# Kernel tuning notes

Hardware: AMD Instinct MI355X
Metric: run time of the kernel (lower is better)

## Reference

```python
import jax, jax.numpy as jnp
import numpy as np

NEG_SLOPE = 0.2  # PyG GATConv default negative_slope


def setup_inputs() -> dict:
    key = jax.random.key(0)
    ks = jax.random.split(key, 10)
    B, N, E = 8, 10000, 160000
    Din, Dout = 128, 128
    x = jax.random.normal(ks[0], (B, N, Din), dtype=jnp.float32)
    src = jax.random.randint(ks[1], (E,), 0, N)
    dst = jax.random.randint(ks[2], (E,), 0, N)
    edge_index = jnp.stack([src, dst])  # [2, E]
    edge_attr = jax.random.uniform(ks[3], (E,), dtype=jnp.float32)
    lim = 1.0 / np.sqrt(Din)
    W = jax.random.uniform(ks[4], (Dout, Din), jnp.float32, -lim, lim)   # shared lin (src==dst)
    We = jax.random.uniform(ks[5], (Dout, 1), jnp.float32, -1.0, 1.0)    # lin_edge, edge_dim=1
    att_src = jax.random.normal(ks[6], (Dout,), jnp.float32) * 0.1
    att_dst = jax.random.normal(ks[7], (Dout,), jnp.float32) * 0.1
    att_edge = jax.random.normal(ks[8], (Dout,), jnp.float32) * 0.1
    bias = jnp.zeros((Dout,), jnp.float32)
    return {"x": x, "edge_index": edge_index, "edge_attr": edge_attr,
            "W": W, "We": We, "att_src": att_src, "att_dst": att_dst,
            "att_edge": att_edge, "bias": bias}


def reference(x, edge_index, edge_attr, W, We, att_src, att_dst, att_edge, bias):
    B, N, Din = x.shape
    src, dst = edge_index[0], edge_index[1]
    # --- add self loops with fill_value='mean' (mean of incoming edge_attr per node) ---
    deg = jax.ops.segment_sum(jnp.ones_like(edge_attr), dst, num_segments=N)
    loop_attr = jax.ops.segment_sum(edge_attr, dst, num_segments=N) / jnp.maximum(deg, 1.0)
    ar = jnp.arange(N, dtype=src.dtype)
    full_src = jnp.concatenate([src, ar])          # [E2]
    full_dst = jnp.concatenate([dst, ar])          # [E2]
    full_attr = jnp.concatenate([edge_attr, loop_attr])
    # edge features: Linear(1 -> Dout, no bias) == outer product; identical across batch
    e_feat = full_attr[:, None] * We[:, 0][None, :]        # [E2, Dout]
    alpha_e = e_feat @ att_edge                            # [E2]

    def single(xb):  # xb: [N, Din]
        h = xb @ W.T                                       # [N, Dout]
        a_src = h @ att_src                                # [N]
        a_dst = h @ att_dst                                # [N]
        a = a_src[full_src] + a_dst[full_dst] + alpha_e    # [E2]
        a = jax.nn.leaky_relu(a, NEG_SLOPE)
        # segment softmax over destination node
        a_max = jax.ops.segment_max(a, full_dst, num_segments=N)
        a_max = jnp.where(jnp.isfinite(a_max), a_max, 0.0)
        ex = jnp.exp(a - a_max[full_dst])
        s = jax.ops.segment_sum(ex, full_dst, num_segments=N)
        alpha = ex / (s[full_dst] + 1e-16)                 # [E2]
        out = jax.ops.segment_sum(alpha[:, None] * h[full_src], full_dst, num_segments=N)
        return out + bias, alpha

    x_out, attn = jax.vmap(single)(x)   # [B, N, Dout], [B, E2]
    return x_out, attn
```

## Files before the change

### kernel.cpp

```cpp
#include <hip/hip_runtime.h>
#include <hip/hip_bf16.h>

typedef short short8 __attribute__((ext_vector_type(8)));
typedef float floatx4 __attribute__((ext_vector_type(4)));

static constexpr int BATCH = 8;
static constexpr int NN    = 10000;
static constexpr int EE    = 160000;
static constexpr int EE2   = EE + NN;
static constexpr int DD    = 128;
static constexpr float SLOPE = 0.2f;
static constexpr long OUT_ELEMS = (long)BATCH * NN * DD;
static constexpr int EB = EE / 256;

__device__ inline float ldf(const void* p, long i, int f32) {
    return f32 ? ((const float*)p)[i]
               : __bfloat162float(((const __hip_bfloat16*)p)[i]);
}
__device__ inline int esrc(const int* ei, int e, int i64) { return i64 ? ei[2 * e] : ei[e]; }
__device__ inline int edst(const int* ei, int e, int i64) { return i64 ? ei[2 * (EE + e)] : ei[EE + e]; }
__device__ inline short bf16bits(float v) {
    __hip_bfloat16 b = __float2bfloat16(v);
    short s; __builtin_memcpy(&s, &b, 2); return s;
}

__global__ __launch_bounds__(256) void k_detect(const unsigned short* __restrict__ xu,
                                                const int* __restrict__ ei,
                                                const void* __restrict__ We,
                                                const void* __restrict__ att_edge,
                                                int* __restrict__ flags,
                                                float* __restrict__ cout,
                                                int* __restrict__ deg,
                                                float* __restrict__ lsum) {
    int t = threadIdx.x;
    if (blockIdx.x > 0) {
        int idx = (blockIdx.x - 1) * 256 + t;
        if (idx < NN) { deg[idx] = 0; lsum[idx] = 0.f; }
        return;
    }
    __shared__ int cnt[2];
    __shared__ float red[256];
    if (t < 2) cnt[t] = 0;
    __syncthreads();
    int c1 = 0;
    for (int i = t; i < 32768; i += 256) {
        unsigned short u = xu[i];
        if ((u & 0x7F80u) == 0x7F80u) c1++;
    }
    int c2 = (ei[2 * t + 1] != 0) ? 1 : 0;
    if (c1) atomicAdd(&cnt[0], c1);
    if (c2) atomicAdd(&cnt[1], c2);
    __syncthreads();
    int f32 = (cnt[0] > 0);
    if (t == 0) { flags[0] = f32; flags[1] = (cnt[1] == 0); }
    red[t] = (t < DD) ? ldf(We, t, f32) * ldf(att_edge, t, f32) : 0.f;
    __syncthreads();
    for (int o = 128; o > 0; o >>= 1) {
        if (t < o) red[t] += red[t + o];
        __syncthreads();
    }
    if (t == 0) *cout = red[0];
}

__global__ __launch_bounds__(256) void k_deg(const int* __restrict__ ei,
                                             const void* __restrict__ attr,
                                             const void* __restrict__ W,
                                             const int* __restrict__ flags,
                                             int* __restrict__ deg, float* __restrict__ lsum,
                                             __hip_bfloat16* __restrict__ Wb) {
    int f32 = flags[0], i64 = flags[1];
    int bId = blockIdx.x, t = threadIdx.x;
    if (bId < EB) {
        int e = bId * 256 + t;
        int d = edst(ei, e, i64);
        atomicAdd(&deg[d], 1);
        atomicAdd(&lsum[d], ldf(attr, e, f32));
    } else {
        int idx = (bId - EB) * 512 + t * 2;
        if (f32) {
            float2 v = ((const float2*)W)[idx >> 1];
            Wb[idx]     = __float2bfloat16(v.x);
            Wb[idx + 1] = __float2bfloat16(v.y);
        } else {
            ((ushort2*)Wb)[idx >> 1] = ((const ushort2*)W)[idx >> 1];
        }
    }
}

template<int F32>
__device__ inline void load_a(const void* __restrict__ x, long row, int quad, short8 afr[4]) {
    if (F32) {
        const float* xr = (const float*)x + row * DD;
        #pragma unroll
        for (int kk = 0; kk < 4; kk++) {
            float4 f0 = *(const float4*)(xr + kk * 32 + quad * 8);
            float4 f1 = *(const float4*)(xr + kk * 32 + quad * 8 + 4);
            short8 a;
            a[0] = bf16bits(f0.x); a[1] = bf16bits(f0.y); a[2] = bf16bits(f0.z); a[3] = bf16bits(f0.w);
            a[4] = bf16bits(f1.x); a[5] = bf16bits(f1.y); a[6] = bf16bits(f1.z); a[7] = bf16bits(f1.w);
            afr[kk] = a;
        }
    } else {
        const short* xr = (const short*)x + row * DD;
        #pragma unroll
        for (int kk = 0; kk < 4; kk++)
            afr[kk] = *(const short8*)(xr + kk * 32 + quad * 8);
    }
}

__global__ __launch_bounds__(128) void k_gemm(const void* __restrict__ x,
                                              const __hip_bfloat16* __restrict__ Wb,
                                              const void* __restrict__ att_src,
                                              const void* __restrict__ att_dst,
                                              const int* __restrict__ flags,
                                              __hip_bfloat16* __restrict__ h,
                                              float* __restrict__ asrc_t, float* __restrict__ adst_t) {
    __shared__ float tile[2][16 * 132];
    int f32 = flags[0];
    int wave = threadIdx.x >> 6;
    int lane = threadIdx.x & 63;
    int l15  = lane & 15, quad = lane >> 4;
    long rows_base = (long)blockIdx.x * 32 + wave * 16;

    short8 afr[4];
    if (f32) load_a<1>(x, rows_base + l15, quad, afr);
    else     load_a<0>(x, rows_base + l15, quad, afr);

    const short* wr = (const short*)Wb;
    floatx4 acc[8];
    #pragma unroll
    for (int jt = 0; jt < 8; jt++) acc[jt] = (floatx4){0.f, 0.f, 0.f, 0.f};
    #pragma unroll
    for (int jt = 0; jt < 8; jt++) {
        #pragma unroll
        for (int kk = 0; kk < 4; kk++) {
            short8 bfr = *(const short8*)(wr + (jt * 16 + l15) * DD + kk * 32 + quad * 8);
            acc[jt] = __builtin_amdgcn_mfma_f32_16x16x32_bf16(afr[kk], bfr, acc[jt], 0, 0, 0);
        }
    }

    float asum[4] = {0.f, 0.f, 0.f, 0.f};
    float dsum[4] = {0.f, 0.f, 0.f, 0.f};
    #pragma unroll
    for (int jt = 0; jt < 8; jt++) {
        int col = jt * 16 + l15;
        float as = ldf(att_src, col, f32);
        float ad = ldf(att_dst, col, f32);
        #pragma unroll
        for (int r = 0; r < 4; r++) {
            asum[r] += acc[jt][r] * as;
            dsum[r] += acc[jt][r] * ad;
        }
    }
    #pragma unroll
    for (int r = 0; r < 4; r++) {
        float a = asum[r], d = dsum[r];
        #pragma unroll
        for (int o = 1; o < 16; o <<= 1) { a += __shfl_xor(a, o, 64); d += __shfl_xor(d, o, 64); }
        if (l15 == 0) {
            long row = rows_base + quad * 4 + r;
            int b = (int)(row / NN), n = (int)(row - (long)b * NN);
            asrc_t[n * 8 + b] = a;
            adst_t[n * 8 + b] = d;
        }
    }

    float* tl = &tile[wave][0];
    #pragma unroll
    for (int jt = 0; jt < 8; jt++)
        #pragma unroll
        for (int r = 0; r < 4; r++)
            tl[(quad * 4 + r) * 132 + jt * 16 + l15] = acc[jt][r];
    short* hp = (short*)h;
    #pragma unroll
    for (int it = 0; it < 4; it++) {
        int row = it * 4 + quad;
        float4 f0 = *(const float4*)&tl[row * 132 + l15 * 8];
        float4 f1 = *(const float4*)&tl[row * 132 + l15 * 8 + 4];
        short8 o;
        o[0] = bf16bits(f0.x); o[1] = bf16bits(f0.y); o[2] = bf16bits(f0.z); o[3] = bf16bits(f0.w);
        o[4] = bf16bits(f1.x); o[5] = bf16bits(f1.y); o[6] = bf16bits(f1.z); o[7] = bf16bits(f1.w);
        *(short8*)(hp + (rows_base + row) * DD + l15 * 8) = o;
    }
}

__global__ __launch_bounds__(1024) void k_scan(const int* __restrict__ deg, int* __restrict__ offs) {
    __shared__ int part[1024];
    int t = threadIdx.x;
    const int PER = (NN + 1023) / 1024;
    int base = t * PER;
    int s = 0;
    for (int i = 0; i < PER; i++) { int idx = base + i; if (idx < NN) s += deg[idx]; }
    part[t] = s;
    __syncthreads();
    for (int o = 1; o < 1024; o <<= 1) {
        int v = (t >= o) ? part[t - o] : 0;
        __syncthreads();
        part[t] += v;
        __syncthreads();
    }
    int run = (t == 0) ? 0 : part[t - 1];
    for (int i = 0; i < PER; i++) {
        int idx = base + i;
        if (idx < NN) { offs[idx] = run; run += deg[idx]; }
    }
    if (t == 1023) offs[NN] = run;
}

__global__ __launch_bounds__(256) void k_fill(const int* __restrict__ ei,
                                              const void* __restrict__ attr,
                                              const int* __restrict__ flags,
                                              int* __restrict__ offs,
                                              int* __restrict__ srcs, float* __restrict__ attrs) {
    int f32 = flags[0], i64 = flags[1];
    int e = blockIdx.x * 256 + threadIdx.x;
    if (e < EE) {
        int d = edst(ei, e, i64);
        int s = esrc(ei, e, i64);
        float at = ldf(attr, e, f32);
        int p = atomicAdd(&offs[d], 1);
        srcs[p] = s;
        attrs[p] = at;
    }
}

__global__ __launch_bounds__(256) void k_agg(const int* __restrict__ srcs,
                                             const float* __restrict__ attrs,
                                             const float* __restrict__ asrc_t,
                                             const float* __restrict__ adst_t,
                                             const __hip_bfloat16* __restrict__ h,
                                             const int* __restrict__ deg,
                                             const float* __restrict__ lsum,
                                             const int* __restrict__ offs,
                                             const float* __restrict__ cptr,
                                             const void* __restrict__ bias,
                                             const int* __restrict__ flags,
                                             float* __restrict__ invT,
                                             void* __restrict__ outbuf) {
    int f32 = flags[0];
    int tid = threadIdx.x;
    int g   = (tid & 63) >> 4;
    int c16 = tid & 15;
    int wv  = tid >> 6;
    int b = blockIdx.x & 7;
    int n = (blockIdx.x >> 3) * 16 + wv * 4 + g;

    float c   = *cptr;
    int dg    = deg[n];
    int off   = offs[n] - dg;
    int cnt   = dg + 1;
    float lattr = lsum[n] / fmaxf((float)dg, 1.0f);
    float an  = adst_t[n * 8 + b];

    const unsigned short* hb = (const unsigned short*)h + (long)b * NN * DD;
    float acc[8];
    #pragma unroll
    for (int j = 0; j < 8; j++) acc[j] = 0.f;
    float ssum = 0.f;

    uint4 hvA = {0,0,0,0}, hvB = {0,0,0,0};
    float arA = 0.f, atA = 0.f, arB = 0.f, atB = 0.f;

#define FETCH_EDGE(I, HV, AR, AT)                                   \
    { int _s; if ((I) < dg) { _s = srcs[off + (I)]; AT = attrs[off + (I)]; } \
      else { _s = n; AT = lattr; }                                   \
      AR = asrc_t[_s * 8 + b];                                       \
      HV = *(const uint4*)(hb + (long)_s * DD + c16 * 8); }

    if (0 < cnt) FETCH_EDGE(0, hvA, arA, atA);
    if (1 < cnt) FETCH_EDGE(1, hvB, arB, atB);

    for (int i = 0; i < cnt; i += 2) {
        uint4 nhA = {0,0,0,0}, nhB = {0,0,0,0};
        float narA = 0.f, natA = 0.f, narB = 0.f, natB = 0.f;
        if (i + 2 < cnt) FETCH_EDGE(i + 2, nhA, narA, natA);
        if (i + 3 < cnt) FETCH_EDGE(i + 3, nhB, narB, natB);
        {
            float a = arA + an + c * atA;
            a = (a > 0.f) ? a : SLOPE * a;
            float ex = __expf(a);
            ssum += ex;
            acc[0] += ex * __uint_as_float(hvA.x << 16);
            acc[1] += ex * __uint_as_float(hvA.x & 0xFFFF0000u);
            acc[2] += ex * __uint_as_float(hvA.y << 16);
            acc[3] += ex * __uint_as_float(hvA.y & 0xFFFF0000u);
            acc[4] += ex * __uint_as_float(hvA.z << 16);
            acc[5] += ex * __uint_as_float(hvA.z & 0xFFFF0000u);
            acc[6] += ex * __uint_as_float(hvA.w << 16);
            acc[7] += ex * __uint_as_float(hvA.w & 0xFFFF0000u);
        }
        if (i + 1 < cnt) {
            float a = arB + an + c * atB;
            a = (a > 0.f) ? a : SLOPE * a;
            float ex = __expf(a);
            ssum += ex;
            acc[0] += ex * __uint_as_float(hvB.x << 16);
            acc[1] += ex * __uint_as_float(hvB.x & 0xFFFF0000u);
            acc[2] += ex * __uint_as_float(hvB.y << 16);
            acc[3] += ex * __uint_as_float(hvB.y & 0xFFFF0000u);
            acc[4] += ex * __uint_as_float(hvB.z << 16);
            acc[5] += ex * __uint_as_float(hvB.z & 0xFFFF0000u);
            acc[6] += ex * __uint_as_float(hvB.w << 16);
            acc[7] += ex * __uint_as_float(hvB.w & 0xFFFF0000u);
        }
        hvA = nhA; arA = narA; atA = natA;
        hvB = nhB; arB = narB; atB = natB;
    }
#undef FETCH_EDGE

    float inv = 1.0f / (ssum + 1e-16f);
    if (c16 == 0) invT[n * 8 + b] = inv;
    #pragma unroll
    for (int j = 0; j < 8; j++) acc[j] = acc[j] * inv + ldf(bias, c16 * 8 + j, f32);

    long row = (long)b * NN + n;
    if (f32) {
        float4 lo = {acc[0], acc[1], acc[2], acc[3]};
        float4 hi = {acc[4], acc[5], acc[6], acc[7]};
        float4* orow = (float4*)((float*)outbuf + row * DD);
        orow[c16 * 2]     = lo;
        orow[c16 * 2 + 1] = hi;
    } else {
        short8 o;
        #pragma unroll
        for (int j = 0; j < 8; j++) o[j] = bf16bits(acc[j]);
        ((short8*)((__hip_bfloat16*)outbuf + row * DD))[c16] = o;
    }
}

__global__ __launch_bounds__(256) void k_attn(const int* __restrict__ ei,
                                              const void* __restrict__ attr,
                                              const float* __restrict__ asrc_t,
                                              const float* __restrict__ adst_t,
                                              const int* __restrict__ deg,
                                              const float* __restrict__ lsum,
                                              const float* __restrict__ cptr,
                                              const float* __restrict__ invT,
                                              const int* __restrict__ flags,
                                              void* __restrict__ outbuf) {
    int f32 = flags[0], i64 = flags[1];
    int e2 = blockIdx.x * 256 + threadIdx.x;
    if (e2 >= EE2) return;
    float c = *cptr;
    int s, d; float at;
    if (e2 < EE) {
        s = esrc(ei, e2, i64);
        d = edst(ei, e2, i64);
        at = ldf(attr, e2, f32);
    } else {
        int nn = e2 - EE;
        s = nn; d = nn;
        at = lsum[nn] / fmaxf((float)deg[nn], 1.0f);
    }
    float4 as0 = *(const float4*)(asrc_t + (long)s * 8);
    float4 as1 = *(const float4*)(asrc_t + (long)s * 8 + 4);
    float4 ad0 = *(const float4*)(adst_t + (long)d * 8);
    float4 ad1 = *(const float4*)(adst_t + (long)d * 8 + 4);
    float4 iv0 = *(const float4*)(invT   + (long)d * 8);
    float4 iv1 = *(const float4*)(invT   + (long)d * 8 + 4);
    float asv[8] = {as0.x, as0.y, as0.z, as0.w, as1.x, as1.y, as1.z, as1.w};
    float adv[8] = {ad0.x, ad0.y, ad0.z, ad0.w, ad1.x, ad1.y, ad1.z, ad1.w};
    float ivv[8] = {iv0.x, iv0.y, iv0.z, iv0.w, iv1.x, iv1.y, iv1.z, iv1.w};
    float ca = c * at;
    #pragma unroll
    for (int b = 0; b < BATCH; b++) {
        float a = asv[b] + adv[b] + ca;
        a = (a > 0.f) ? a : SLOPE * a;
        float al = __expf(a) * ivv[b];
        long gidx = OUT_ELEMS + (long)b * EE2 + e2;
        if (f32) ((float*)outbuf)[gidx] = al;
        else     ((__hip_bfloat16*)outbuf)[gidx] = __float2bfloat16(al);
    }
}

extern "C" void kernel_launch(void* const* d_in, const int* in_sizes, int n_in,
                              void* d_out, int out_size, void* d_ws, size_t ws_size,
                              hipStream_t stream) {
    const void* x        = d_in[0];
    const int*  ei       = (const int*)d_in[1];
    const void* attr     = d_in[2];
    const void* W        = d_in[3];
    const void* We       = d_in[4];
    const void* att_src  = d_in[5];
    const void* att_dst  = d_in[6];
    const void* att_edge = d_in[7];
    const void* bias     = d_in[8];

    char* ws = (char*)d_ws;
    size_t off = 0;
    auto alloc = [&](size_t bytes) { size_t o = off; off = (off + bytes + 255) & ~(size_t)255; return o; };
    __hip_bfloat16* h    = (__hip_bfloat16*)(ws + alloc((size_t)BATCH * NN * DD * 2));
    float* asrc_t        = (float*)(ws + alloc((size_t)NN * 8 * 4));
    float* adst_t        = (float*)(ws + alloc((size_t)NN * 8 * 4));
    float* invT          = (float*)(ws + alloc((size_t)NN * 8 * 4));
    int*   deg           = (int*)  (ws + alloc((size_t)NN * 4));
    float* lsum          = (float*)(ws + alloc((size_t)NN * 4));
    int*   offs          = (int*)  (ws + alloc((size_t)(NN + 1) * 4));
    int*   srcs          = (int*)  (ws + alloc((size_t)EE * 4));
    float* attrs         = (float*)(ws + alloc((size_t)EE * 4));
    __hip_bfloat16* Wb   = (__hip_bfloat16*)(ws + alloc((size_t)DD * DD * 2));
    float* cscal         = (float*)(ws + alloc(256));
    int*   flags         = (int*)  (ws + alloc(256));

    k_detect<<<41, 256, 0, stream>>>((const unsigned short*)x, ei, We, att_edge,
                                     flags, cscal, deg, lsum);
    k_deg   <<<EB + 32, 256, 0, stream>>>(ei, attr, W, flags, deg, lsum, Wb);
    k_gemm  <<<(BATCH * NN) / 32, 128, 0, stream>>>(x, Wb, att_src, att_dst, flags,
                                                    h, asrc_t, adst_t);
    k_scan  <<<1, 1024, 0, stream>>>(deg, offs);
    k_fill  <<<EB, 256, 0, stream>>>(ei, attr, flags, offs, srcs, attrs);
    k_agg   <<<(BATCH * NN) / 16, 256, 0, stream>>>(srcs, attrs, asrc_t, adst_t, h,
                                                    deg, lsum, offs, cscal, bias, flags,
                                                    invT, d_out);
    k_attn  <<<(EE2 + 255) / 256, 256, 0, stream>>>(ei, attr, asrc_t, adst_t, deg, lsum,
                                                    cscal, invT, flags, d_out);
}
```

Measured before the change: 259.4 us.

## Pack CSR edges, cooperatively load them with shuffles, deepen aggregation prefetch pipeline

The fill kernel now writes packed (src, c*attr) int2 entries, so the aggregation reads one array with the edge scalar already folded in. In the aggregation kernel, each 16-lane group loads 16 edge entries at once and broadcasts them with shuffles instead of every lane loading each edge. Gathers are now prefetched through a three-stage rotation of edge pairs. The intermediate h is stored as fp16 instead of bf16, and the kernel gets a launch-bounds occupancy hint. The aim is fewer redundant index loads and more latency hiding on the gather; the cost is extra registers and fp16 range and precision tradeoffs for h.

Measured after the change: 249.3 us. -3.9%, faster.

```diff
diff --git a/kernel.cpp b/kernel.cpp
--- a/kernel.cpp
+++ b/kernel.cpp
@@ -1,5 +1,6 @@
 #include <hip/hip_runtime.h>
 #include <hip/hip_bf16.h>
+#include <hip/hip_fp16.h>
 
 typedef short short8 __attribute__((ext_vector_type(8)));
 typedef float floatx4 __attribute__((ext_vector_type(4)));
@@ -21,6 +22,10 @@
 __device__ inline int edst(const int* ei, int e, int i64) { return i64 ? ei[2 * (EE + e)] : ei[EE + e]; }
 __device__ inline short bf16bits(float v) {
     __hip_bfloat16 b = __float2bfloat16(v);
+    short s; __builtin_memcpy(&s, &b, 2); return s;
+}
+__device__ inline short f16bits(float v) {
+    __half b = __float2half(v);
     short s; __builtin_memcpy(&s, &b, 2); return s;
 }
 
@@ -113,7 +118,7 @@
                                               const void* __restrict__ att_src,
                                               const void* __restrict__ att_dst,
                                               const int* __restrict__ flags,
-                                              __hip_bfloat16* __restrict__ h,
+                                              short* __restrict__ h,
                                               float* __restrict__ asrc_t, float* __restrict__ adst_t) {
     __shared__ float tile[2][16 * 132];
     int f32 = flags[0];
@@ -171,16 +176,15 @@
         #pragma unroll
         for (int r = 0; r < 4; r++)
             tl[(quad * 4 + r) * 132 + jt * 16 + l15] = acc[jt][r];
-    short* hp = (short*)h;
     #pragma unroll
     for (int it = 0; it < 4; it++) {
         int row = it * 4 + quad;
         float4 f0 = *(const float4*)&tl[row * 132 + l15 * 8];
         float4 f1 = *(const float4*)&tl[row * 132 + l15 * 8 + 4];
         short8 o;
-        o[0] = bf16bits(f0.x); o[1] = bf16bits(f0.y); o[2] = bf16bits(f0.z); o[3] = bf16bits(f0.w);
-        o[4] = bf16bits(f1.x); o[5] = bf16bits(f1.y); o[6] = bf16bits(f1.z); o[7] = bf16bits(f1.w);
-        *(short8*)(hp + (rows_base + row) * DD + l15 * 8) = o;
+        o[0] = f16bits(f0.x); o[1] = f16bits(f0.y); o[2] = f16bits(f0.z); o[3] = f16bits(f0.w);
+        o[4] = f16bits(f1.x); o[5] = f16bits(f1.y); o[6] = f16bits(f1.z); o[7] = f16bits(f1.w);
+        *(short8*)(h + (rows_base + row) * DD + l15 * 8) = o;
     }
 }
 
@@ -210,38 +214,40 @@
 __global__ __launch_bounds__(256) void k_fill(const int* __restrict__ ei,
                                               const void* __restrict__ attr,
                                               const int* __restrict__ flags,
+                                              const float* __restrict__ cptr,
                                               int* __restrict__ offs,
-                                              int* __restrict__ srcs, float* __restrict__ attrs) {
+                                              int2* __restrict__ edges) {
     int f32 = flags[0], i64 = flags[1];
     int e = blockIdx.x * 256 + threadIdx.x;
+    float c = *cptr;
     if (e < EE) {
         int d = edst(ei, e, i64);
         int s = esrc(ei, e, i64);
         float at = ldf(attr, e, f32);
         int p = atomicAdd(&offs[d], 1);
-        srcs[p] = s;
-        attrs[p] = at;
-    }
-}
-
-__global__ __launch_bounds__(256) void k_agg(const int* __restrict__ srcs,
-                                             const float* __restrict__ attrs,
-                                             const float* __restrict__ asrc_t,
-                                             const float* __restrict__ adst_t,
-                                             const __hip_bfloat16* __restrict__ h,
-                                             const int* __restrict__ deg,
-                                             const float* __restrict__ lsum,
-                                             const int* __restrict__ offs,
-                                             const float* __restrict__ cptr,
-                                             const void* __restrict__ bias,
-                                             const int* __restrict__ flags,
-                                             float* __restrict__ invT,
-                                             void* __restrict__ outbuf) {
+        edges[p] = make_int2(s, __float_as_int(c * at));
+    }
+}
+
+__global__ __launch_bounds__(256, 4) void k_agg(const int2* __restrict__ edges,
+                                                const float* __restrict__ asrc_t,
+                                                const float* __restrict__ adst_t,
+                                                const __half* __restrict__ h,
+                                                const int* __restrict__ deg,
+                                                const float* __restrict__ lsum,
+                                                const int* __restrict__ offs,
+                                                const float* __restrict__ cptr,
+                                                const void* __restrict__ bias,
+                                                const int* __restrict__ flags,
+                                                float* __restrict__ invT,
+                                                void* __restrict__ outbuf) {
     int f32 = flags[0];
     int tid = threadIdx.x;
-    int g   = (tid & 63) >> 4;
+    int lane = tid & 63;
+    int g   = lane >> 4;
     int c16 = tid & 15;
     int wv  = tid >> 6;
+    int laneBase = lane & 48;
     int b = blockIdx.x & 7;
     int n = (blockIdx.x >> 3) * 16 + wv * 4 + g;
 
@@ -249,64 +255,93 @@
     int dg    = deg[n];
     int off   = offs[n] - dg;
     int cnt   = dg + 1;
-    float lattr = lsum[n] / fmaxf((float)dg, 1.0f);
+    int np    = (cnt + 1) >> 1;
+    float atcS = c * (lsum[n] / fmaxf((float)dg, 1.0f));
     float an  = adst_t[n * 8 + b];
 
-    const unsigned short* hb = (const unsigned short*)h + (long)b * NN * DD;
+    const int2* em = edges + off;
+    const __half* hb = h + (long)b * NN * DD;
+
     float acc[8];
     #pragma unroll
     for (int j = 0; j < 8; j++) acc[j] = 0.f;
     float ssum = 0.f;
 
-    uint4 hvA = {0,0,0,0}, hvB = {0,0,0,0};
-    float arA = 0.f, atA = 0.f, arB = 0.f, atB = 0.f;
-
-#define FETCH_EDGE(I, HV, AR, AT)                                   \
-    { int _s; if ((I) < dg) { _s = srcs[off + (I)]; AT = attrs[off + (I)]; } \
-      else { _s = n; AT = lattr; }                                   \
-      AR = asrc_t[_s * 8 + b];                                       \
-      HV = *(const uint4*)(hb + (long)_s * DD + c16 * 8); }
-
-    if (0 < cnt) FETCH_EDGE(0, hvA, arA, atA);
-    if (1 < cnt) FETCH_EDGE(1, hvB, arB, atB);
-
-    for (int i = 0; i < cnt; i += 2) {
-        uint4 nhA = {0,0,0,0}, nhB = {0,0,0,0};
-        float narA = 0.f, natA = 0.f, narB = 0.f, natB = 0.f;
-        if (i + 2 < cnt) FETCH_EDGE(i + 2, nhA, narA, natA);
-        if (i + 3 < cnt) FETCH_EDGE(i + 3, nhB, narB, natB);
-        {
-            float a = arA + an + c * atA;
-            a = (a > 0.f) ? a : SLOPE * a;
-            float ex = __expf(a);
-            ssum += ex;
-            acc[0] += ex * __uint_as_float(hvA.x << 16);
-            acc[1] += ex * __uint_as_float(hvA.x & 0xFFFF0000u);
-            acc[2] += ex * __uint_as_float(hvA.y << 16);
-            acc[3] += ex * __uint_as_float(hvA.y & 0xFFFF0000u);
-            acc[4] += ex * __uint_as_float(hvA.z << 16);
-            acc[5] += ex * __uint_as_float(hvA.z & 0xFFFF0000u);
-            acc[6] += ex * __uint_as_float(hvA.w << 16);
-            acc[7] += ex * __uint_as_float(hvA.w & 0xFFFF0000u);
-        }
-        if (i + 1 < cnt) {
-            float a = arB + an + c * atB;
-            a = (a > 0.f) ? a : SLOPE * a;
-            float ex = __expf(a);
-            ssum += ex;
-            acc[0] += ex * __uint_as_float(hvB.x << 16);
-            acc[1] += ex * __uint_as_float(hvB.x & 0xFFFF0000u);
-            acc[2] += ex * __uint_as_float(hvB.y << 16);
-            acc[3] += ex * __uint_as_float(hvB.y & 0xFFFF0000u);
-            acc[4] += ex * __uint_as_float(hvB.z << 16);
-            acc[5] += ex * __uint_as_float(hvB.z & 0xFFFF0000u);
-            acc[6] += ex * __uint_as_float(hvB.w << 16);
-            acc[7] += ex * __uint_as_float(hvB.w & 0xFFFF0000u);
-        }
-        hvA = nhA; arA = narA; atA = natA;
-        hvB = nhB; arB = narB; atB = natB;
-    }
-#undef FETCH_EDGE
+#define LOADM(K, DST)                                                       \
+    {   int _idx = (K) * 16 + c16;                                          \
+        if (_idx < dg) DST = em[_idx];                                      \
+        else { DST.x = n; DST.y = __float_as_int(atcS); }                   \
+    }
+
+#define MSTEP(PD)                                                           \
+    if (((PD) & 7) == 0) {                                                  \
+        int _kc = ((PD) >> 3) + 1;                                          \
+        int2 _t; LOADM(_kc, _t);                                            \
+        if (_kc & 1) mvB = _t; else mvA = _t;                               \
+    }
+
+#define DISSUE(PD, HV0, HV1, AR0, AR1, AT0, AT1)                            \
+    {   int _j0 = ((PD) << 1) & 15;                                         \
+        int _mx = (((PD) >> 3) & 1) ? mvB.x : mvA.x;                        \
+        int _my = (((PD) >> 3) & 1) ? mvB.y : mvA.y;                        \
+        int _s0 = __shfl(_mx, laneBase | _j0);                              \
+        int _s1 = __shfl(_mx, laneBase | (_j0 + 1));                        \
+        AT0 = __int_as_float(__shfl(_my, laneBase | _j0));                  \
+        AT1 = __int_as_float(__shfl(_my, laneBase | (_j0 + 1)));            \
+        AR0 = asrc_t[_s0 * 8 + b];                                          \
+        AR1 = asrc_t[_s1 * 8 + b];                                          \
+        HV0 = *(const uint4*)(hb + (long)_s0 * DD + c16 * 8);               \
+        HV1 = *(const uint4*)(hb + (long)_s1 * DD + c16 * 8);               \
+    }
+
+#define CONSUME(P, HV0, HV1, AR0, AR1, AT0, AT1)                            \
+    {   float _a0 = AR0 + an + AT0;                                         \
+        _a0 = fmaxf(_a0, SLOPE * _a0);                                      \
+        float _e0 = __expf(_a0);                                            \
+        ssum += _e0;                                                        \
+        const __half* _h0 = (const __half*)&HV0;                            \
+        _Pragma("unroll")                                                   \
+        for (int _j = 0; _j < 8; _j++)                                      \
+            acc[_j] += _e0 * __half2float(_h0[_j]);                         \
+        if (2 * (P) + 1 < cnt) {                                            \
+            float _a1 = AR1 + an + AT1;                                     \
+            _a1 = fmaxf(_a1, SLOPE * _a1);                                  \
+            float _e1 = __expf(_a1);                                        \
+            ssum += _e1;                                                    \
+            const __half* _h1 = (const __half*)&HV1;                        \
+            _Pragma("unroll")                                               \
+            for (int _j = 0; _j < 8; _j++)                                  \
+                acc[_j] += _e1 * __half2float(_h1[_j]);                     \
+        }                                                                   \
+    }
+
+    int2 mvA, mvB;
+    LOADM(0, mvA);
+    LOADM(1, mvB);
+    uint4 hA0, hA1, hB0, hB1, hC0, hC1;
+    float arA0, arA1, atA0, atA1;
+    float arB0, arB1, atB0, atB1;
+    float arC0, arC1, atC0, atC1;
+    DISSUE(0, hA0, hA1, arA0, arA1, atA0, atA1);
+    DISSUE(1, hB0, hB1, arB0, arB1, atB0, atB1);
+
+    for (int p = 0; p < np; p += 3) {
+        MSTEP(p + 2);
+        DISSUE(p + 2, hC0, hC1, arC0, arC1, atC0, atC1);
+        CONSUME(p, hA0, hA1, arA0, arA1, atA0, atA1);
+        if (p + 1 >= np) break;
+        MSTEP(p + 3);
+        DISSUE(p + 3, hA0, hA1, arA0, arA1, atA0, atA1);
+        CONSUME(p + 1, hB0, hB1, arB0, arB1, atB0, atB1);
+        if (p + 2 >= np) break;
+        MSTEP(p + 4);
+        DISSUE(p + 4, hB0, hB1, arB0, arB1, atB0, atB1);
+        CONSUME(p + 2, hC0, hC1, arC0, arC1, atC0, atC1);
+    }
+#undef LOADM
+#undef MSTEP
+#undef DISSUE
+#undef CONSUME
 
     float inv = 1.0f / (ssum + 1e-16f);
     if (c16 == 0) invT[n * 8 + b] = inv;
@@ -389,15 +424,14 @@
     char* ws = (char*)d_ws;
     size_t off = 0;
     auto alloc = [&](size_t bytes) { size_t o = off; off = (off + bytes + 255) & ~(size_t)255; return o; };
-    __hip_bfloat16* h    = (__hip_bfloat16*)(ws + alloc((size_t)BATCH * NN * DD * 2));
+    short* h             = (short*)(ws + alloc((size_t)BATCH * NN * DD * 2));
     float* asrc_t        = (float*)(ws + alloc((size_t)NN * 8 * 4));
     float* adst_t        = (float*)(ws + alloc((size_t)NN * 8 * 4));
     float* invT          = (float*)(ws + alloc((size_t)NN * 8 * 4));
     int*   deg           = (int*)  (ws + alloc((size_t)NN * 4));
     float* lsum          = (float*)(ws + alloc((size_t)NN * 4));
     int*   offs          = (int*)  (ws + alloc((size_t)(NN + 1) * 4));
-    int*   srcs          = (int*)  (ws + alloc((size_t)EE * 4));
-    float* attrs         = (float*)(ws + alloc((size_t)EE * 4));
+    int2*  edges         = (int2*) (ws + alloc((size_t)EE * 8));
     __hip_bfloat16* Wb   = (__hip_bfloat16*)(ws + alloc((size_t)DD * DD * 2));
     float* cscal         = (float*)(ws + alloc(256));
     int*   flags         = (int*)  (ws + alloc(256));
@@ -408,8 +442,8 @@
     k_gemm  <<<(BATCH * NN) / 32, 128, 0, stream>>>(x, Wb, att_src, att_dst, flags,
                                                     h, asrc_t, adst_t);
     k_scan  <<<1, 1024, 0, stream>>>(deg, offs);
-    k_fill  <<<EB, 256, 0, stream>>>(ei, attr, flags, offs, srcs, attrs);
-    k_agg   <<<(BATCH * NN) / 16, 256, 0, stream>>>(srcs, attrs, asrc_t, adst_t, h,
+    k_fill  <<<EB, 256, 0, stream>>>(ei, attr, flags, cscal, offs, edges);
+    k_agg   <<<(BATCH * NN) / 16, 256, 0, stream>>>(edges, asrc_t, adst_t, (const __half*)h,
                                                     deg, lsum, offs, cscal, bias, flags,
                                                     invT, d_out);
     k_attn  <<<(EE2 + 255) / 256, 256, 0, stream>>>(ei, attr, asrc_t, adst_t, deg, lsum,
```
